# Kernel optimization log

Measured on AMD Instinct MI355X. Metric: run time of the kernel, lower is better.

Reference implementation:

```python
import jax, jax.numpy as jnp
import numpy as np

B, S, D, H, DH, TLEN, TD = 4, 1024, 1024, 16, 64, 256, 256
EPS = 1e-5


def layer_norm(x, g, b):
    m = jnp.mean(x, axis=-1, keepdims=True)
    v = jnp.mean((x - m) ** 2, axis=-1, keepdims=True)
    return (x - m) * jax.lax.rsqrt(v + EPS) * g + b


def rotate_half(x):
    x1, x2 = jnp.split(x, 2, axis=-1)
    return jnp.concatenate((-x2, x1), axis=-1)


def apply_rope(pos, t):
    # pos: [S, DH] -> [1, S, 1, DH]; t: [B, S, H, DH]
    p = pos[None, :, None, :]
    return t * jnp.cos(p) + rotate_half(t) * jnp.sin(p)


def mha(q_in, kv_in, in_w, in_b, out_w, out_b, n_heads):
    # standard nn.MultiheadAttention math (batch-first tensors here)
    d = q_in.shape[-1]
    dh = d // n_heads
    q = q_in @ in_w[:d].T + in_b[:d]
    k = kv_in @ in_w[d:2 * d].T + in_b[d:2 * d]
    v = kv_in @ in_w[2 * d:].T + in_b[2 * d:]
    q = q.reshape(q.shape[0], q.shape[1], n_heads, dh)
    k = k.reshape(k.shape[0], k.shape[1], n_heads, dh)
    v = v.reshape(v.shape[0], v.shape[1], n_heads, dh)
    scores = jnp.einsum('bihd,bjhd->bhij', q, k) / jnp.sqrt(jnp.asarray(dh, q.dtype))
    attn = jax.nn.softmax(scores, axis=-1)
    o = jnp.einsum('bhij,bjhd->bihd', attn, v)
    o = o.reshape(o.shape[0], o.shape[1], d)
    return o @ out_w.T + out_b


def setup_inputs():
    key = jax.random.key(0)
    ks = jax.random.split(key, 20)
    s = 0.02
    inp = {
        'x': jax.random.normal(ks[0], (B, S, D), jnp.float32),
        'text_emb': jax.random.normal(ks[1], (B, TLEN, D), jnp.float32),
        'time_emb': jax.random.normal(ks[2], (B, TD), jnp.float32),
    }
    # true RoPE position encoding, matching RotaryEmbedding.forward
    inv_freq = 1.0 / (10000 ** (jnp.arange(0, DH, 2, dtype=jnp.float32) / DH))
    freqs = jnp.arange(S, dtype=jnp.float32)[:, None] * inv_freq[None, :]
    inp['rotary_pos'] = jnp.concatenate((freqs, freqs), axis=-1)  # [S, DH]
    inp.update(
        ln1_g=jnp.ones((D,), jnp.float32), ln1_b=jnp.zeros((D,), jnp.float32),
        ln2_g=jnp.ones((D,), jnp.float32), ln2_b=jnp.zeros((D,), jnp.float32),
        ln3_g=jnp.ones((D,), jnp.float32), ln3_b=jnp.zeros((D,), jnp.float32),
        attn_in_w=jax.random.normal(ks[3], (3 * D, D), jnp.float32) * s,
        attn_in_b=jnp.zeros((3 * D,), jnp.float32),
        ca_in_w=jax.random.normal(ks[4], (3 * D, D), jnp.float32) * s,
        ca_in_b=jnp.zeros((3 * D,), jnp.float32),
        ca_out_w=jax.random.normal(ks[5], (D, D), jnp.float32) * s,
        ca_out_b=jnp.zeros((D,), jnp.float32),
        fc1_w=jax.random.normal(ks[6], (4 * D, D), jnp.float32) * s,
        fc1_b=jnp.zeros((4 * D,), jnp.float32),
        gate_w=jax.random.normal(ks[7], (4 * D, D), jnp.float32) * s,
        gate_b=jnp.zeros((4 * D,), jnp.float32),
        fc2_w=jax.random.normal(ks[8], (D, 4 * D), jnp.float32) * s,
        fc2_b=jnp.zeros((D,), jnp.float32),
    )
    return inp


def reference(x, text_emb, time_emb, rotary_pos,
              ln1_g, ln1_b, ln2_g, ln2_b, ln3_g, ln3_b,
              attn_in_w, attn_in_b,
              ca_in_w, ca_in_b, ca_out_w, ca_out_b,
              fc1_w, fc1_b, gate_w, gate_b, fc2_w, fc2_b):
    b, n, d = x.shape
    # --- self-attention with manual RoPE (NOTE: original skips out_proj) ---
    residual = x
    xn = layer_norm(x, ln1_g, ln1_b)
    q = xn @ attn_in_w[:d].T + attn_in_b[:d]
    k = xn @ attn_in_w[d:2 * d].T + attn_in_b[d:2 * d]
    v = xn @ attn_in_w[2 * d:].T + attn_in_b[2 * d:]
    q = q.reshape(b, n, H, DH)
    k = k.reshape(b, n, H, DH)
    v = v.reshape(b, n, H, DH)
    q = apply_rope(rotary_pos, q)
    k = apply_rope(rotary_pos, k)
    scores = jnp.einsum('bihd,bjhd->bhij', q, k) / jnp.sqrt(jnp.asarray(DH, x.dtype))
    attn = jax.nn.softmax(scores, axis=-1)
    attn_out = jnp.einsum('bhij,bjhd->bihd', attn, v).reshape(b, n, d)
    x = attn_out + residual
    # --- cross-attention (full MHA, dropout inactive at eval) ---
    residual = x
    xn = layer_norm(x, ln2_g, ln2_b)
    x = mha(xn, text_emb, ca_in_w, ca_in_b, ca_out_w, ca_out_b, H) + residual
    # --- gated MLP ---
    residual = x
    xn = layer_norm(x, ln3_g, ln3_b)
    h = jax.nn.gelu(xn @ fc1_w.T + fc1_b, approximate=False)
    g = jax.nn.sigmoid(xn @ gate_w.T + gate_b)
    return (h * g) @ fc2_w.T + fc2_b + residual
```

## Files before the change

### kernel.cpp

```cpp
#include <hip/hip_runtime.h>
#include <hip/hip_bf16.h>

#define SEQ 1024
#define DIM 1024
#define NH 16

typedef __bf16 bf16_t;
typedef __bf16 bf16x8 __attribute__((ext_vector_type(8)));
typedef __bf16 bf16x4 __attribute__((ext_vector_type(4)));
typedef float f32x4 __attribute__((ext_vector_type(4)));

__device__ __forceinline__ f32x4 mfma16(bf16x8 a, bf16x8 b, f32x4 c) {
    return __builtin_amdgcn_mfma_f32_16x16x32_bf16(a, b, c, 0, 0, 0);
}

__device__ __forceinline__ void gload16(const bf16_t* g, bf16_t* l) {
    __builtin_amdgcn_global_load_lds(
        (const __attribute__((address_space(1))) void*)g,
        (__attribute__((address_space(3))) void*)l, 16, 0, 0);
}

__global__ __launch_bounds__(256) void cvt_kernel(const float* __restrict__ in,
                                                  bf16_t* __restrict__ out) {
    const int i = blockIdx.x * 256 + threadIdx.x;
    const float4 v = ((const float4*)in)[i];
    bf16x4 o = {(bf16_t)v.x, (bf16_t)v.y, (bf16_t)v.z, (bf16_t)v.w};
    ((bf16x4*)out)[i] = o;
}

__global__ __launch_bounds__(256) void ln_kernel(const float* __restrict__ in,
                                                 const float* __restrict__ g,
                                                 const float* __restrict__ bsh,
                                                 bf16_t* __restrict__ out) {
    __shared__ float red[4], red2[4];
    const int row = blockIdx.x, tid = threadIdx.x;
    const float4 v = ((const float4*)(in + (size_t)row * DIM))[tid];
    float s = v.x + v.y + v.z + v.w;
#pragma unroll
    for (int o = 32; o; o >>= 1) s += __shfl_down(s, o, 64);
    if ((tid & 63) == 0) red[tid >> 6] = s;
    __syncthreads();
    const float mean = (red[0] + red[1] + red[2] + red[3]) * (1.0f / DIM);
    const float dx = v.x - mean, dy = v.y - mean, dz = v.z - mean, dw = v.w - mean;
    float s2 = dx * dx + dy * dy + dz * dz + dw * dw;
#pragma unroll
    for (int o = 32; o; o >>= 1) s2 += __shfl_xor(s2, o, 64);
    if ((tid & 63) == 0) red2[tid >> 6] = s2;
    __syncthreads();
    const float var = (red2[0] + red2[1] + red2[2] + red2[3]) * (1.0f / DIM);
    const float rs = rsqrtf(var + 1e-5f);
    const float4 gv = ((const float4*)g)[tid];
    const float4 bv = ((const float4*)bsh)[tid];
    bf16x4 o4 = {(bf16_t)(dx * rs * gv.x + bv.x), (bf16_t)(dy * rs * gv.y + bv.y),
                 (bf16_t)(dz * rs * gv.z + bv.z), (bf16_t)(dw * rs * gv.w + bv.w)};
    ((bf16x4*)(out + (size_t)row * DIM))[tid] = o4;
}

__global__ __launch_bounds__(256) void rope_kernel(bf16_t* __restrict__ qkv,
                                                   const float* __restrict__ rp) {
    const int t = blockIdx.x * 256 + threadIdx.x;
    const int row = t >> 9;
    const int rem = t & 511;
    const int h = rem >> 5, d = rem & 31;
    const int s = row & (SEQ - 1);
    const float p0 = rp[s * 64 + d];
    const float p1 = rp[s * 64 + d + 32];
    float s0, c0, s1, c1;
    sincosf(p0, &s0, &c0);
    sincosf(p1, &s1, &c1);
    const size_t base = (size_t)row * 3072 + h * 64 + d;
#pragma unroll
    for (int off = 0; off <= 1024; off += 1024) {
        const float a = (float)qkv[base + off];
        const float b = (float)qkv[base + off + 32];
        qkv[base + off] = (bf16_t)(a * c0 - b * s0);
        qkv[base + off + 32] = (bf16_t)(b * c1 + a * s1);
    }
}

enum { EPI_BF16 = 0, EPI_F32_RESID = 1, EPI_BF16_GELU = 2, EPI_BF16_SIGMUL = 3 };

template <int EPI>
__global__ __launch_bounds__(256) void gemm_bf16(
    const bf16_t* __restrict__ A, int lda, const bf16_t* __restrict__ W, int ldw,
    const float* __restrict__ bias, const void* __restrict__ aux,
    void* __restrict__ outv, int ldo, int K) {
    __shared__ bf16_t As[128 * 32];
    __shared__ bf16_t Bs[128 * 32];
    const int tid = threadIdx.x;
    const int wave = tid >> 6, lane = tid & 63;
    const int wr = wave >> 1, wc = wave & 1;
    const int lr = lane & 15, hi = lane >> 4;

    const int gy = gridDim.y;
    int lin = blockIdx.x * gy + blockIdx.y;
    const int cpx = (gridDim.x * gy) >> 3;
    lin = (lin & 7) * cpx + (lin >> 3);
    const int rowB0 = (lin / gy) * 128;
    const int rowA0 = (lin % gy) * 128;

    const int sr = lane >> 2, sc = (lane & 3) * 8;

    f32x4 acc[4][4];
#pragma unroll
    for (int m = 0; m < 4; ++m)
#pragma unroll
        for (int n = 0; n < 4; ++n) acc[m][n] = (f32x4){0.f, 0.f, 0.f, 0.f};

    for (int k0 = 0; k0 < K; k0 += 32) {
        const bf16_t* Ag = A + (size_t)(rowA0) * lda + k0;
        const bf16_t* Bg = W + (size_t)(rowB0) * ldw + k0;
#pragma unroll
        for (int t = 0; t < 2; ++t) {
            const int ci = wave * 2 + t;
            gload16(Ag + (size_t)(ci * 16 + sr) * lda + sc, As + ci * 512);
            gload16(Bg + (size_t)(ci * 16 + sr) * ldw + sc, Bs + ci * 512);
        }
        __syncthreads();
        bf16x8 af[4], bfr[4];
#pragma unroll
        for (int m = 0; m < 4; ++m)
            af[m] = *(const bf16x8*)&As[(wr * 64 + m * 16 + lr) * 32 + hi * 8];
#pragma unroll
        for (int n = 0; n < 4; ++n)
            bfr[n] = *(const bf16x8*)&Bs[(wc * 64 + n * 16 + lr) * 32 + hi * 8];
#pragma unroll
        for (int m = 0; m < 4; ++m)
#pragma unroll
            for (int n = 0; n < 4; ++n) acc[m][n] = mfma16(af[m], bfr[n], acc[m][n]);
        __syncthreads();
    }

    float bn[4];
#pragma unroll
    for (int n = 0; n < 4; ++n) bn[n] = bias[rowB0 + wc * 64 + n * 16 + lr];
#pragma unroll
    for (int m = 0; m < 4; ++m) {
#pragma unroll
        for (int j = 0; j < 4; ++j) {
            const int row = rowA0 + wr * 64 + m * 16 + hi * 4 + j;
#pragma unroll
            for (int n = 0; n < 4; ++n) {
                const int col = rowB0 + wc * 64 + n * 16 + lr;
                float val = acc[m][n][j] + bn[n];
                const size_t oidx = (size_t)row * ldo + col;
                if constexpr (EPI == EPI_BF16) {
                    ((bf16_t*)outv)[oidx] = (bf16_t)val;
                } else if constexpr (EPI == EPI_F32_RESID) {
                    ((float*)outv)[oidx] = val + ((const float*)aux)[oidx];
                } else if constexpr (EPI == EPI_BF16_GELU) {
                    ((bf16_t*)outv)[oidx] =
                        (bf16_t)(0.5f * val * (1.0f + erff(val * 0.70710678118f)));
                } else {
                    const float sg = 1.0f / (1.0f + expf(-val));
                    ((bf16_t*)outv)[oidx] =
                        (bf16_t)(sg * (float)((const bf16_t*)aux)[oidx]);
                }
            }
        }
    }
}

#define ALD 72
template <bool OUTBF>
__global__ __launch_bounds__(256) void attn_kernel(
    const bf16_t* __restrict__ qp, int ldq, int qoff,
    const bf16_t* __restrict__ kp, int ldk, int koff,
    const bf16_t* __restrict__ vp, int ldv, int voff, int skv,
    const float* __restrict__ resid, void* __restrict__ outp, float scale) {
    __shared__ bf16_t Ks[64 * ALD];
    __shared__ bf16_t Vt[64 * ALD];
    __shared__ bf16_t Ps[4 * 16 * ALD];
    const int b = blockIdx.z, h = blockIdx.y, qt = blockIdx.x;
    const int tid = threadIdx.x;
    const int wave = tid >> 6, lane = tid & 63;
    const int lr = lane & 15, hi = lane >> 4;

    const size_t qrow = (size_t)(b * SEQ + qt * 64 + wave * 16 + lr);
    const bf16_t* qb = qp + qrow * ldq + qoff + h * 64;
    const bf16x8 qf0 = *(const bf16x8*)(qb + hi * 8);
    const bf16x8 qf1 = *(const bf16x8*)(qb + 32 + hi * 8);

    f32x4 oacc[4];
#pragma unroll
    for (int n = 0; n < 4; ++n) oacc[n] = (f32x4){0.f, 0.f, 0.f, 0.f};
    float mrun[4] = {-1e30f, -1e30f, -1e30f, -1e30f};
    float lrun[4] = {0.f, 0.f, 0.f, 0.f};

    bf16_t* pw = &Ps[wave * 16 * ALD];
    const int nkt = skv >> 6;
    for (int kt = 0; kt < nkt; ++kt) {
#pragma unroll
        for (int t = 0; t < 2; ++t) {
            const int idx = t * 256 + tid;
            const int key = idx >> 3, c8 = (idx & 7) * 8;
            const size_t krow = (size_t)(b * skv + kt * 64 + key);
            bf16x8 kv = *(const bf16x8*)(kp + krow * ldk + koff + h * 64 + c8);
            *(bf16x8*)&Ks[key * ALD + c8] = kv;
            bf16x8 vv = *(const bf16x8*)(vp + krow * ldv + voff + h * 64 + c8);
#pragma unroll
            for (int i = 0; i < 8; ++i) Vt[(c8 + i) * ALD + key] = vv[i];
        }
        __syncthreads();

        f32x4 s[4];
#pragma unroll
        for (int n = 0; n < 4; ++n) {
            f32x4 z = (f32x4){0.f, 0.f, 0.f, 0.f};
            z = mfma16(qf0, *(const bf16x8*)&Ks[(n * 16 + lr) * ALD + hi * 8], z);
            z = mfma16(qf1, *(const bf16x8*)&Ks[(n * 16 + lr) * ALD + 32 + hi * 8], z);
            s[n] = z * scale;
        }
        float alpha[4];
#pragma unroll
        for (int j = 0; j < 4; ++j) {
            float mt = fmaxf(fmaxf(s[0][j], s[1][j]), fmaxf(s[2][j], s[3][j]));
#pragma unroll
            for (int o = 8; o >= 1; o >>= 1) mt = fmaxf(mt, __shfl_xor(mt, o, 64));
            const float mnew = fmaxf(mrun[j], mt);
            alpha[j] = expf(mrun[j] - mnew);
            float rsum = 0.f;
#pragma unroll
            for (int n = 0; n < 4; ++n) {
                const float p = expf(s[n][j] - mnew);
                s[n][j] = p;
                rsum += p;
            }
#pragma unroll
            for (int o = 8; o >= 1; o >>= 1) rsum += __shfl_xor(rsum, o, 64);
            lrun[j] = lrun[j] * alpha[j] + rsum;
            mrun[j] = mnew;
        }
#pragma unroll
        for (int j = 0; j < 4; ++j) {
            const int pr = hi * 4 + j;
#pragma unroll
            for (int n = 0; n < 4; ++n) pw[pr * ALD + n * 16 + lr] = (bf16_t)s[n][j];
        }
#pragma unroll
        for (int n = 0; n < 4; ++n)
#pragma unroll
            for (int j = 0; j < 4; ++j) oacc[n][j] *= alpha[j];
#pragma unroll
        for (int ks = 0; ks < 2; ++ks) {
            const bf16x8 pa = *(const bf16x8*)&pw[lr * ALD + ks * 32 + hi * 8];
#pragma unroll
            for (int n = 0; n < 4; ++n) {
                const bf16x8 vf = *(const bf16x8*)&Vt[(n * 16 + lr) * ALD + ks * 32 + hi * 8];
                oacc[n] = mfma16(pa, vf, oacc[n]);
            }
        }
        __syncthreads();
    }

    const size_t orow0 = (size_t)(b * SEQ + qt * 64 + wave * 16);
#pragma unroll
    for (int n = 0; n < 4; ++n) {
#pragma unroll
        for (int j = 0; j < 4; ++j) {
            const int r = hi * 4 + j;
            const size_t idx = (orow0 + r) * DIM + h * 64 + n * 16 + lr;
            float val = oacc[n][j] / lrun[j];
            if constexpr (OUTBF) {
                ((bf16_t*)outp)[idx] = (bf16_t)val;
            } else {
                ((float*)outp)[idx] = val + resid[idx];
            }
        }
    }
}

extern "C" void kernel_launch(void* const* d_in, const int* in_sizes, int n_in,
                              void* d_out, int out_size, void* d_ws, size_t ws_size,
                              hipStream_t stream) {
    const float* x = (const float*)d_in[0];
    const float* text_emb = (const float*)d_in[1];
    const float* rotary = (const float*)d_in[3];
    const float* ln1_g = (const float*)d_in[4];
    const float* ln1_b = (const float*)d_in[5];
    const float* ln2_g = (const float*)d_in[6];
    const float* ln2_b = (const float*)d_in[7];
    const float* ln3_g = (const float*)d_in[8];
    const float* ln3_b = (const float*)d_in[9];
    const float* attn_in_w = (const float*)d_in[10];
    const float* attn_in_b = (const float*)d_in[11];
    const float* ca_in_w = (const float*)d_in[12];
    const float* ca_in_b = (const float*)d_in[13];
    const float* ca_out_w = (const float*)d_in[14];
    const float* ca_out_b = (const float*)d_in[15];
    const float* fc1_w = (const float*)d_in[16];
    const float* fc1_b = (const float*)d_in[17];
    const float* gate_w = (const float*)d_in[18];
    const float* gate_b = (const float*)d_in[19];
    const float* fc2_w = (const float*)d_in[20];
    const float* fc2_b = (const float*)d_in[21];

    char* ws = (char*)d_ws;
    bf16_t* attn_w_bf = (bf16_t*)(ws);
    bf16_t* ca_in_bf = (bf16_t*)(ws + 6291456);
    bf16_t* ca_out_bf = (bf16_t*)(ws + 12582912);
    bf16_t* fc1_bf = (bf16_t*)(ws + 14680064);
    bf16_t* gate_bf = (bf16_t*)(ws + 23068672);
    bf16_t* fc2_bf = (bf16_t*)(ws + 31457280);
    bf16_t* text_bf = (bf16_t*)(ws + 39845888);
    bf16_t* xn = (bf16_t*)(ws + 41943040);
    float* xA = (float*)(ws + 50331648);
    char* S = ws + 67108864;
    bf16_t* qkv = (bf16_t*)S;
    bf16_t* cq = (bf16_t*)S;
    bf16_t* ckv = (bf16_t*)(S + 8388608);
    bf16_t* ca_attn = (bf16_t*)(S + 12582912);
    bf16_t* hbuf = (bf16_t*)S;
    float* out = (float*)d_out;

    cvt_kernel<<<3072, 256, 0, stream>>>(attn_in_w, attn_w_bf);
    cvt_kernel<<<3072, 256, 0, stream>>>(ca_in_w, ca_in_bf);
    cvt_kernel<<<1024, 256, 0, stream>>>(ca_out_w, ca_out_bf);
    cvt_kernel<<<4096, 256, 0, stream>>>(fc1_w, fc1_bf);
    cvt_kernel<<<4096, 256, 0, stream>>>(gate_w, gate_bf);
    cvt_kernel<<<4096, 256, 0, stream>>>(fc2_w, fc2_bf);
    cvt_kernel<<<1024, 256, 0, stream>>>(text_emb, text_bf);

    ln_kernel<<<4096, 256, 0, stream>>>(x, ln1_g, ln1_b, xn);
    gemm_bf16<EPI_BF16><<<dim3(24, 32), 256, 0, stream>>>(
        xn, 1024, attn_w_bf, 1024, attn_in_b, nullptr, qkv, 3072, 1024);
    rope_kernel<<<8192, 256, 0, stream>>>(qkv, rotary);
    attn_kernel<false><<<dim3(16, 16, 4), 256, 0, stream>>>(
        qkv, 3072, 0, qkv, 3072, 1024, qkv, 3072, 2048, 1024, x, xA, 0.125f);

    ln_kernel<<<4096, 256, 0, stream>>>(xA, ln2_g, ln2_b, xn);
    gemm_bf16<EPI_BF16><<<dim3(8, 32), 256, 0, stream>>>(
        xn, 1024, ca_in_bf, 1024, ca_in_b, nullptr, cq, 1024, 1024);
    gemm_bf16<EPI_BF16><<<dim3(16, 8), 256, 0, stream>>>(
        text_bf, 1024, ca_in_bf + (size_t)1024 * 1024, 1024, ca_in_b + 1024, nullptr,
        ckv, 2048, 1024);
    attn_kernel<true><<<dim3(16, 16, 4), 256, 0, stream>>>(
        cq, 1024, 0, ckv, 2048, 0, ckv, 2048, 1024, 256, nullptr, ca_attn, 0.125f);
    gemm_bf16<EPI_F32_RESID><<<dim3(8, 32), 256, 0, stream>>>(
        ca_attn, 1024, ca_out_bf, 1024, ca_out_b, xA, xA, 1024, 1024);

    ln_kernel<<<4096, 256, 0, stream>>>(xA, ln3_g, ln3_b, xn);
    gemm_bf16<EPI_BF16_GELU><<<dim3(32, 32), 256, 0, stream>>>(
        xn, 1024, fc1_bf, 1024, fc1_b, nullptr, hbuf, 4096, 1024);
    gemm_bf16<EPI_BF16_SIGMUL><<<dim3(32, 32), 256, 0, stream>>>(
        xn, 1024, gate_bf, 1024, gate_b, hbuf, hbuf, 4096, 1024);
    gemm_bf16<EPI_F32_RESID><<<dim3(8, 32), 256, 0, stream>>>(
        hbuf, 4096, fc2_bf, 4096, fc2_b, xA, out, 1024, 4096);
}
```

Measured before the change: 533.9 us.

## Add double-buffered 256x256-tile GEMM for QKV, fc1 and gate projections

Adds a gemm256 kernel with 512 threads, a 256x256 output tile, K-step 64 and double-buffered LDS staging through global_load_lds. It also raises MFMA priority with s_setprio. The existing 128-tile GEMM is changed to double-buffer its LDS tiles, so the next k-slice loads while the current one computes. The QKV, fc1 and gate projections now use the larger tile to get more data reuse per block and fewer global loads. The trade-off is fewer blocks (192 or 256) on a large-CU GPU, high register pressure from 32 accumulators per thread, and an empty stub epi_store function left in.

```diff
diff --git a/kernel.cpp b/kernel.cpp
--- a/kernel.cpp
+++ b/kernel.cpp
@@ -18,6 +18,12 @@
     __builtin_amdgcn_global_load_lds(
         (const __attribute__((address_space(1))) void*)g,
         (__attribute__((address_space(3))) void*)l, 16, 0, 0);
+}
+
+enum { EPI_BF16 = 0, EPI_F32_RESID = 1, EPI_BF16_GELU = 2, EPI_BF16_SIGMUL = 3 };
+
+__device__ __forceinline__ void epi_store(int EPI_, void* outv, size_t oidx,
+                                          float val, const void* aux) {
 }
 
 __global__ __launch_bounds__(256) void cvt_kernel(const float* __restrict__ in,
@@ -78,15 +84,13 @@
     }
 }
 
-enum { EPI_BF16 = 0, EPI_F32_RESID = 1, EPI_BF16_GELU = 2, EPI_BF16_SIGMUL = 3 };
-
 template <int EPI>
 __global__ __launch_bounds__(256) void gemm_bf16(
     const bf16_t* __restrict__ A, int lda, const bf16_t* __restrict__ W, int ldw,
     const float* __restrict__ bias, const void* __restrict__ aux,
     void* __restrict__ outv, int ldo, int K) {
-    __shared__ bf16_t As[128 * 32];
-    __shared__ bf16_t Bs[128 * 32];
+    __shared__ bf16_t As[2][4096];
+    __shared__ bf16_t Bs[2][4096];
     const int tid = threadIdx.x;
     const int wave = tid >> 6, lane = tid & 63;
     const int wr = wave >> 1, wc = wave & 1;
@@ -107,23 +111,30 @@
 #pragma unroll
         for (int n = 0; n < 4; ++n) acc[m][n] = (f32x4){0.f, 0.f, 0.f, 0.f};
 
-    for (int k0 = 0; k0 < K; k0 += 32) {
-        const bf16_t* Ag = A + (size_t)(rowA0) * lda + k0;
-        const bf16_t* Bg = W + (size_t)(rowB0) * ldw + k0;
+    auto stage = [&](int kt, int b) {
+        const bf16_t* Ag = A + (size_t)rowA0 * lda + kt * 32;
+        const bf16_t* Bg = W + (size_t)rowB0 * ldw + kt * 32;
 #pragma unroll
         for (int t = 0; t < 2; ++t) {
             const int ci = wave * 2 + t;
-            gload16(Ag + (size_t)(ci * 16 + sr) * lda + sc, As + ci * 512);
-            gload16(Bg + (size_t)(ci * 16 + sr) * ldw + sc, Bs + ci * 512);
-        }
-        __syncthreads();
+            gload16(Ag + (size_t)(ci * 16 + sr) * lda + sc, &As[b][ci * 512]);
+            gload16(Bg + (size_t)(ci * 16 + sr) * ldw + sc, &Bs[b][ci * 512]);
+        }
+    };
+
+    stage(0, 0);
+    __syncthreads();
+    const int NT = K >> 5;
+    for (int kt = 0; kt < NT; ++kt) {
+        const int b = kt & 1;
+        if (kt + 1 < NT) stage(kt + 1, b ^ 1);
         bf16x8 af[4], bfr[4];
 #pragma unroll
         for (int m = 0; m < 4; ++m)
-            af[m] = *(const bf16x8*)&As[(wr * 64 + m * 16 + lr) * 32 + hi * 8];
+            af[m] = *(const bf16x8*)&As[b][(wr * 64 + m * 16 + lr) * 32 + hi * 8];
 #pragma unroll
         for (int n = 0; n < 4; ++n)
-            bfr[n] = *(const bf16x8*)&Bs[(wc * 64 + n * 16 + lr) * 32 + hi * 8];
+            bfr[n] = *(const bf16x8*)&Bs[b][(wc * 64 + n * 16 + lr) * 32 + hi * 8];
 #pragma unroll
         for (int m = 0; m < 4; ++m)
 #pragma unroll
@@ -142,6 +153,115 @@
 #pragma unroll
             for (int n = 0; n < 4; ++n) {
                 const int col = rowB0 + wc * 64 + n * 16 + lr;
+                float val = acc[m][n][j] + bn[n];
+                const size_t oidx = (size_t)row * ldo + col;
+                if constexpr (EPI == EPI_BF16) {
+                    ((bf16_t*)outv)[oidx] = (bf16_t)val;
+                } else if constexpr (EPI == EPI_F32_RESID) {
+                    ((float*)outv)[oidx] = val + ((const float*)aux)[oidx];
+                } else if constexpr (EPI == EPI_BF16_GELU) {
+                    ((bf16_t*)outv)[oidx] =
+                        (bf16_t)(0.5f * val * (1.0f + erff(val * 0.70710678118f)));
+                } else {
+                    const float sg = 1.0f / (1.0f + expf(-val));
+                    ((bf16_t*)outv)[oidx] =
+                        (bf16_t)(sg * (float)((const bf16_t*)aux)[oidx]);
+                }
+            }
+        }
+    }
+}
+
+template <int EPI>
+__global__ __launch_bounds__(512, 1) void gemm256(
+    const bf16_t* __restrict__ A, int lda, const bf16_t* __restrict__ W, int ldw,
+    const float* __restrict__ bias, const void* __restrict__ aux,
+    void* __restrict__ outv, int ldo, int K) {
+    __shared__ bf16_t As[2][2][8192];
+    __shared__ bf16_t Bs[2][2][8192];
+    const int tid = threadIdx.x;
+    const int wave = tid >> 6, lane = tid & 63;
+    const int wm = wave >> 2, wn = wave & 3;
+    const int lr = lane & 15, hi = lane >> 4;
+
+    const int gy = gridDim.y;
+    int lin = blockIdx.x * gy + blockIdx.y;
+    const int cpx = (gridDim.x * gy) >> 3;
+    lin = (lin & 7) * cpx + (lin >> 3);
+    const int rowB0 = (lin / gy) * 256;
+    const int rowA0 = (lin % gy) * 256;
+
+    const int srow = wave * 16 + (lane >> 2);
+    const int scol = (lane & 3) * 8;
+
+    f32x4 acc[8][4];
+#pragma unroll
+    for (int m = 0; m < 8; ++m)
+#pragma unroll
+        for (int n = 0; n < 4; ++n) acc[m][n] = (f32x4){0.f, 0.f, 0.f, 0.f};
+
+    auto stage = [&](int kt, int b) {
+        const size_t koff = (size_t)kt * 64;
+#pragma unroll
+        for (int h = 0; h < 2; ++h) {
+#pragma unroll
+            for (int i = 0; i < 2; ++i) {
+                gload16(A + (size_t)(rowA0 + h * 128 + srow) * lda + koff + i * 32 + scol,
+                        &As[b][h][i * 4096 + wave * 512]);
+                gload16(W + (size_t)(rowB0 + h * 128 + srow) * ldw + koff + i * 32 + scol,
+                        &Bs[b][h][i * 4096 + wave * 512]);
+            }
+        }
+    };
+
+    stage(0, 0);
+    __syncthreads();
+    const int NT = K >> 6;
+    const int bh = wn >> 1, bg0 = (wn & 1) * 4;
+    for (int kt = 0; kt < NT; ++kt) {
+        const int b = kt & 1;
+        if (kt + 1 < NT) stage(kt + 1, b ^ 1);
+#pragma unroll
+        for (int p = 0; p < 4; ++p) {
+            const int qm = p >> 1, qn = p & 1;
+            bf16x8 af[4][2], bfr[2][2];
+#pragma unroll
+            for (int mf = 0; mf < 4; ++mf)
+#pragma unroll
+                for (int ks = 0; ks < 2; ++ks)
+                    af[mf][ks] = *(const bf16x8*)&As[b][wm][(ks * 8 + qm * 4 + mf) * 512 +
+                                                           lr * 32 + hi * 8];
+#pragma unroll
+            for (int nf = 0; nf < 2; ++nf)
+#pragma unroll
+                for (int ks = 0; ks < 2; ++ks)
+                    bfr[nf][ks] = *(const bf16x8*)&Bs[b][bh][(ks * 8 + bg0 + qn * 2 + nf) * 512 +
+                                                            lr * 32 + hi * 8];
+            __builtin_amdgcn_s_setprio(1);
+#pragma unroll
+            for (int mf = 0; mf < 4; ++mf)
+#pragma unroll
+                for (int nf = 0; nf < 2; ++nf)
+#pragma unroll
+                    for (int ks = 0; ks < 2; ++ks)
+                        acc[qm * 4 + mf][qn * 2 + nf] =
+                            mfma16(af[mf][ks], bfr[nf][ks], acc[qm * 4 + mf][qn * 2 + nf]);
+            __builtin_amdgcn_s_setprio(0);
+        }
+        __syncthreads();
+    }
+
+    float bn[4];
+#pragma unroll
+    for (int n = 0; n < 4; ++n) bn[n] = bias[rowB0 + wn * 64 + n * 16 + lr];
+#pragma unroll
+    for (int m = 0; m < 8; ++m) {
+#pragma unroll
+        for (int j = 0; j < 4; ++j) {
+            const int row = rowA0 + wm * 128 + m * 16 + hi * 4 + j;
+#pragma unroll
+            for (int n = 0; n < 4; ++n) {
+                const int col = rowB0 + wn * 64 + n * 16 + lr;
                 float val = acc[m][n][j] + bn[n];
                 const size_t oidx = (size_t)row * ldo + col;
                 if constexpr (EPI == EPI_BF16) {
@@ -322,7 +442,7 @@
     cvt_kernel<<<1024, 256, 0, stream>>>(text_emb, text_bf);
 
     ln_kernel<<<4096, 256, 0, stream>>>(x, ln1_g, ln1_b, xn);
-    gemm_bf16<EPI_BF16><<<dim3(24, 32), 256, 0, stream>>>(
+    gemm256<EPI_BF16><<<dim3(12, 16), 512, 0, stream>>>(
         xn, 1024, attn_w_bf, 1024, attn_in_b, nullptr, qkv, 3072, 1024);
     rope_kernel<<<8192, 256, 0, stream>>>(qkv, rotary);
     attn_kernel<false><<<dim3(16, 16, 4), 256, 0, stream>>>(
@@ -340,9 +460,9 @@
         ca_attn, 1024, ca_out_bf, 1024, ca_out_b, xA, xA, 1024, 1024);
 
     ln_kernel<<<4096, 256, 0, stream>>>(xA, ln3_g, ln3_b, xn);
-    gemm_bf16<EPI_BF16_GELU><<<dim3(32, 32), 256, 0, stream>>>(
+    gemm256<EPI_BF16_GELU><<<dim3(16, 16), 512, 0, stream>>>(
         xn, 1024, fc1_bf, 1024, fc1_b, nullptr, hbuf, 4096, 1024);
-    gemm_bf16<EPI_BF16_SIGMUL><<<dim3(32, 32), 256, 0, stream>>>(
+    gemm256<EPI_BF16_SIGMUL><<<dim3(16, 16), 512, 0, stream>>>(
         xn, 1024, gate_bf, 1024, gate_b, hbuf, hbuf, 4096, 1024);
     gemm_bf16<EPI_F32_RESID><<<dim3(8, 32), 256, 0, stream>>>(
         hbuf, 4096, fc2_bf, 4096, fc2_b, xA, out, 1024, 4096);
```

Result: slower. 588.7 us (+10.3%).

## Double-buffer GEMM LDS tiles with async prefetch two stages ahead

Applied to the files above, without the earlier changes.

Converts the bf16 GEMM main loop from a single LDS buffer with load-then-sync to a two-buffer pipeline. The tile two k-steps ahead is issued via global_load_lds while the current tile is consumed, with explicit vmcnt waits and barriers. It also raises wave priority around the MFMA block. The goal is to hide global-load latency behind MFMA work, at the cost of doubled LDS use and hand-managed wait counts that must match the number of outstanding loads.

```diff
diff --git a/kernel.cpp b/kernel.cpp
--- a/kernel.cpp
+++ b/kernel.cpp
@@ -19,6 +19,8 @@
         (const __attribute__((address_space(1))) void*)g,
         (__attribute__((address_space(3))) void*)l, 16, 0, 0);
 }
+
+enum { EPI_BF16 = 0, EPI_F32_RESID = 1, EPI_BF16_GELU = 2, EPI_BF16_SIGMUL = 3 };
 
 __global__ __launch_bounds__(256) void cvt_kernel(const float* __restrict__ in,
                                                   bf16_t* __restrict__ out) {
@@ -78,15 +80,13 @@
     }
 }
 
-enum { EPI_BF16 = 0, EPI_F32_RESID = 1, EPI_BF16_GELU = 2, EPI_BF16_SIGMUL = 3 };
-
 template <int EPI>
 __global__ __launch_bounds__(256) void gemm_bf16(
     const bf16_t* __restrict__ A, int lda, const bf16_t* __restrict__ W, int ldw,
     const float* __restrict__ bias, const void* __restrict__ aux,
     void* __restrict__ outv, int ldo, int K) {
-    __shared__ bf16_t As[128 * 32];
-    __shared__ bf16_t Bs[128 * 32];
+    __shared__ bf16_t As[2][4096];
+    __shared__ bf16_t Bs[2][4096];
     const int tid = threadIdx.x;
     const int wave = tid >> 6, lane = tid & 63;
     const int wr = wave >> 1, wc = wave & 1;
@@ -107,28 +107,49 @@
 #pragma unroll
         for (int n = 0; n < 4; ++n) acc[m][n] = (f32x4){0.f, 0.f, 0.f, 0.f};
 
-    for (int k0 = 0; k0 < K; k0 += 32) {
-        const bf16_t* Ag = A + (size_t)(rowA0) * lda + k0;
-        const bf16_t* Bg = W + (size_t)(rowB0) * ldw + k0;
+    auto stage = [&](int kt, int b) {
+        const bf16_t* Ag = A + (size_t)rowA0 * lda + kt * 32;
+        const bf16_t* Bg = W + (size_t)rowB0 * ldw + kt * 32;
 #pragma unroll
         for (int t = 0; t < 2; ++t) {
             const int ci = wave * 2 + t;
-            gload16(Ag + (size_t)(ci * 16 + sr) * lda + sc, As + ci * 512);
-            gload16(Bg + (size_t)(ci * 16 + sr) * ldw + sc, Bs + ci * 512);
-        }
-        __syncthreads();
+            gload16(Ag + (size_t)(ci * 16 + sr) * lda + sc, &As[b][ci * 512]);
+            gload16(Bg + (size_t)(ci * 16 + sr) * ldw + sc, &Bs[b][ci * 512]);
+        }
+    };
+
+    const int NT = K >> 5;
+    stage(0, 0);
+    stage(1, 1);
+    asm volatile("s_waitcnt vmcnt(4)" ::: "memory");
+    __builtin_amdgcn_s_barrier();
+
+    for (int kt = 0; kt < NT; ++kt) {
+        const int b = kt & 1;
         bf16x8 af[4], bfr[4];
 #pragma unroll
         for (int m = 0; m < 4; ++m)
-            af[m] = *(const bf16x8*)&As[(wr * 64 + m * 16 + lr) * 32 + hi * 8];
+            af[m] = *(const bf16x8*)&As[b][(wr * 64 + m * 16 + lr) * 32 + hi * 8];
 #pragma unroll
         for (int n = 0; n < 4; ++n)
-            bfr[n] = *(const bf16x8*)&Bs[(wc * 64 + n * 16 + lr) * 32 + hi * 8];
+            bfr[n] = *(const bf16x8*)&Bs[b][(wc * 64 + n * 16 + lr) * 32 + hi * 8];
+        __builtin_amdgcn_s_setprio(1);
 #pragma unroll
         for (int m = 0; m < 4; ++m)
 #pragma unroll
             for (int n = 0; n < 4; ++n) acc[m][n] = mfma16(af[m], bfr[n], acc[m][n]);
-        __syncthreads();
+        __builtin_amdgcn_s_setprio(0);
+        if (kt + 1 < NT) {
+            __builtin_amdgcn_sched_barrier(0);
+            __builtin_amdgcn_s_barrier();
+            if (kt + 2 < NT) {
+                stage(kt + 2, b);
+                asm volatile("s_waitcnt vmcnt(4)" ::: "memory");
+            } else {
+                asm volatile("s_waitcnt vmcnt(0)" ::: "memory");
+            }
+            __builtin_amdgcn_s_barrier();
+        }
     }
 
     float bn[4];
```

After: 574.6 us. 1.08x slower.

## Replace GEMM with 8-wave double-buffered kernel using BK=64 and fragment-friendly LDS layout

Applied to the files above, without the earlier changes.

Replaces the 4-wave 128x128 GEMM with an 8-wave version that double-buffers LDS tiles across K steps of 64, issuing the next stage's async global-to-LDS loads before computing on the current tile. This removes one barrier per iteration and overlaps memory with MFMA work. The LDS layout is also changed so each 16x32 sub-chunk matches the MFMA fragment order, and the tile swizzle becomes a 1D grid mapping. It doubles LDS use to 64KB per block and halves per-wave accumulators, which trades register pressure against occupancy. The single barrier per iteration may also race: the next stage is written into the other buffer while slow waves could still be reading it.

```diff
diff --git a/kernel.cpp b/kernel.cpp
--- a/kernel.cpp
+++ b/kernel.cpp
@@ -19,6 +19,8 @@
         (const __attribute__((address_space(1))) void*)g,
         (__attribute__((address_space(3))) void*)l, 16, 0, 0);
 }
+
+enum { EPI_BF16 = 0, EPI_F32_RESID = 1, EPI_BF16_GELU = 2, EPI_BF16_SIGMUL = 3 };
 
 __global__ __launch_bounds__(256) void cvt_kernel(const float* __restrict__ in,
                                                   bf16_t* __restrict__ out) {
@@ -78,70 +80,83 @@
     }
 }
 
-enum { EPI_BF16 = 0, EPI_F32_RESID = 1, EPI_BF16_GELU = 2, EPI_BF16_SIGMUL = 3 };
+__device__ __forceinline__ float epi_apply_gelu(float v) {
+    return 0.5f * v * (1.0f + erff(v * 0.70710678118f));
+}
 
 template <int EPI>
-__global__ __launch_bounds__(256) void gemm_bf16(
+__global__ __launch_bounds__(512, 4) void gemm8w(
     const bf16_t* __restrict__ A, int lda, const bf16_t* __restrict__ W, int ldw,
     const float* __restrict__ bias, const void* __restrict__ aux,
-    void* __restrict__ outv, int ldo, int K) {
-    __shared__ bf16_t As[128 * 32];
-    __shared__ bf16_t Bs[128 * 32];
+    void* __restrict__ outv, int ldo, int K, int nM) {
+    __shared__ bf16_t As[2][8192];
+    __shared__ bf16_t Bs[2][8192];
     const int tid = threadIdx.x;
     const int wave = tid >> 6, lane = tid & 63;
-    const int wr = wave >> 1, wc = wave & 1;
+    const int wm = wave >> 2, wn = wave & 3;
     const int lr = lane & 15, hi = lane >> 4;
 
-    const int gy = gridDim.y;
-    int lin = blockIdx.x * gy + blockIdx.y;
-    const int cpx = (gridDim.x * gy) >> 3;
-    lin = (lin & 7) * cpx + (lin >> 3);
-    const int rowB0 = (lin / gy) * 128;
-    const int rowA0 = (lin % gy) * 128;
-
-    const int sr = lane >> 2, sc = (lane & 3) * 8;
-
-    f32x4 acc[4][4];
+    const int q = gridDim.x >> 3;
+    const int t = (blockIdx.x & 7) * q + (blockIdx.x >> 3);
+    const int rowA0 = (t % nM) * 128;
+    const int rowB0 = (t / nM) * 128;
+
+    f32x4 acc[4][2];
 #pragma unroll
     for (int m = 0; m < 4; ++m)
 #pragma unroll
-        for (int n = 0; n < 4; ++n) acc[m][n] = (f32x4){0.f, 0.f, 0.f, 0.f};
-
-    for (int k0 = 0; k0 < K; k0 += 32) {
-        const bf16_t* Ag = A + (size_t)(rowA0) * lda + k0;
-        const bf16_t* Bg = W + (size_t)(rowB0) * ldw + k0;
-#pragma unroll
-        for (int t = 0; t < 2; ++t) {
-            const int ci = wave * 2 + t;
-            gload16(Ag + (size_t)(ci * 16 + sr) * lda + sc, As + ci * 512);
-            gload16(Bg + (size_t)(ci * 16 + sr) * ldw + sc, Bs + ci * 512);
+        for (int n = 0; n < 2; ++n) acc[m][n] = (f32x4){0.f, 0.f, 0.f, 0.f};
+
+    const int c0 = wave * 2;
+    auto stage = [&](int kt, int b) {
+        const int k0 = kt * 64;
+#pragma unroll
+        for (int u = 0; u < 2; ++u) {
+            const int c = c0 + u, s = c >> 1, ks = c & 1;
+            const int grow = s * 16 + lr, gcol = k0 + ks * 32 + hi * 8;
+            gload16(A + (size_t)(rowA0 + grow) * lda + gcol, &As[b][c * 512]);
+            gload16(W + (size_t)(rowB0 + grow) * ldw + gcol, &Bs[b][c * 512]);
+        }
+    };
+
+    const int NT = K >> 6;
+    stage(0, 0);
+    __syncthreads();
+
+    for (int kt = 0; kt < NT; ++kt) {
+        const int cur = kt & 1;
+        if (kt + 1 < NT) stage(kt + 1, cur ^ 1);
+#pragma unroll
+        for (int ks = 0; ks < 2; ++ks) {
+            bf16x8 af[4], bfr[2];
+#pragma unroll
+            for (int mf = 0; mf < 4; ++mf)
+                af[mf] = *(const bf16x8*)&As[cur][((wm * 4 + mf) * 2 + ks) * 512 +
+                                                 hi * 128 + lr * 8];
+#pragma unroll
+            for (int nf = 0; nf < 2; ++nf)
+                bfr[nf] = *(const bf16x8*)&Bs[cur][((wn * 2 + nf) * 2 + ks) * 512 +
+                                                  hi * 128 + lr * 8];
+#pragma unroll
+            for (int mf = 0; mf < 4; ++mf)
+#pragma unroll
+                for (int nf = 0; nf < 2; ++nf)
+                    acc[mf][nf] = mfma16(af[mf], bfr[nf], acc[mf][nf]);
         }
         __syncthreads();
-        bf16x8 af[4], bfr[4];
-#pragma unroll
-        for (int m = 0; m < 4; ++m)
-            af[m] = *(const bf16x8*)&As[(wr * 64 + m * 16 + lr) * 32 + hi * 8];
-#pragma unroll
-        for (int n = 0; n < 4; ++n)
-            bfr[n] = *(const bf16x8*)&Bs[(wc * 64 + n * 16 + lr) * 32 + hi * 8];
-#pragma unroll
-        for (int m = 0; m < 4; ++m)
-#pragma unroll
-            for (int n = 0; n < 4; ++n) acc[m][n] = mfma16(af[m], bfr[n], acc[m][n]);
-        __syncthreads();
-    }
-
-    float bn[4];
-#pragma unroll
-    for (int n = 0; n < 4; ++n) bn[n] = bias[rowB0 + wc * 64 + n * 16 + lr];
+    }
+
+    float bn[2];
+#pragma unroll
+    for (int n = 0; n < 2; ++n) bn[n] = bias[rowB0 + wn * 32 + n * 16 + lr];
 #pragma unroll
     for (int m = 0; m < 4; ++m) {
 #pragma unroll
         for (int j = 0; j < 4; ++j) {
-            const int row = rowA0 + wr * 64 + m * 16 + hi * 4 + j;
-#pragma unroll
-            for (int n = 0; n < 4; ++n) {
-                const int col = rowB0 + wc * 64 + n * 16 + lr;
+            const int row = rowA0 + wm * 64 + m * 16 + hi * 4 + j;
+#pragma unroll
+            for (int n = 0; n < 2; ++n) {
+                const int col = rowB0 + wn * 32 + n * 16 + lr;
                 float val = acc[m][n][j] + bn[n];
                 const size_t oidx = (size_t)row * ldo + col;
                 if constexpr (EPI == EPI_BF16) {
@@ -149,8 +164,7 @@
                 } else if constexpr (EPI == EPI_F32_RESID) {
                     ((float*)outv)[oidx] = val + ((const float*)aux)[oidx];
                 } else if constexpr (EPI == EPI_BF16_GELU) {
-                    ((bf16_t*)outv)[oidx] =
-                        (bf16_t)(0.5f * val * (1.0f + erff(val * 0.70710678118f)));
+                    ((bf16_t*)outv)[oidx] = (bf16_t)epi_apply_gelu(val);
                 } else {
                     const float sg = 1.0f / (1.0f + expf(-val));
                     ((bf16_t*)outv)[oidx] =
@@ -322,28 +336,28 @@
     cvt_kernel<<<1024, 256, 0, stream>>>(text_emb, text_bf);
 
     ln_kernel<<<4096, 256, 0, stream>>>(x, ln1_g, ln1_b, xn);
-    gemm_bf16<EPI_BF16><<<dim3(24, 32), 256, 0, stream>>>(
-        xn, 1024, attn_w_bf, 1024, attn_in_b, nullptr, qkv, 3072, 1024);
+    gemm8w<EPI_BF16><<<768, 512, 0, stream>>>(
+        xn, 1024, attn_w_bf, 1024, attn_in_b, nullptr, qkv, 3072, 1024, 32);
     rope_kernel<<<8192, 256, 0, stream>>>(qkv, rotary);
     attn_kernel<false><<<dim3(16, 16, 4), 256, 0, stream>>>(
         qkv, 3072, 0, qkv, 3072, 1024, qkv, 3072, 2048, 1024, x, xA, 0.125f);
 
     ln_kernel<<<4096, 256, 0, stream>>>(xA, ln2_g, ln2_b, xn);
-    gemm_bf16<EPI_BF16><<<dim3(8, 32), 256, 0, stream>>>(
-        xn, 1024, ca_in_bf, 1024, ca_in_b, nullptr, cq, 1024, 1024);
-    gemm_bf16<EPI_BF16><<<dim3(16, 8), 256, 0, stream>>>(
+    gemm8w<EPI_BF16><<<256, 512, 0, stream>>>(
+        xn, 1024, ca_in_bf, 1024, ca_in_b, nullptr, cq, 1024, 1024, 32);
+    gemm8w<EPI_BF16><<<128, 512, 0, stream>>>(
         text_bf, 1024, ca_in_bf + (size_t)1024 * 1024, 1024, ca_in_b + 1024, nullptr,
-        ckv, 2048, 1024);
+        ckv, 2048, 1024, 8);
     attn_kernel<true><<<dim3(16, 16, 4), 256, 0, stream>>>(
         cq, 1024, 0, ckv, 2048, 0, ckv, 2048, 1024, 256, nullptr, ca_attn, 0.125f);
-    gemm_bf16<EPI_F32_RESID><<<dim3(8, 32), 256, 0, stream>>>(
-        ca_attn, 1024, ca_out_bf, 1024, ca_out_b, xA, xA, 1024, 1024);
+    gemm8w<EPI_F32_RESID><<<256, 512, 0, stream>>>(
+        ca_attn, 1024, ca_out_bf, 1024, ca_out_b, xA, xA, 1024, 1024, 32);
 
     ln_kernel<<<4096, 256, 0, stream>>>(xA, ln3_g, ln3_b, xn);
-    gemm_bf16<EPI_BF16_GELU><<<dim3(32, 32), 256, 0, stream>>>(
-        xn, 1024, fc1_bf, 1024, fc1_b, nullptr, hbuf, 4096, 1024);
-    gemm_bf16<EPI_BF16_SIGMUL><<<dim3(32, 32), 256, 0, stream>>>(
-        xn, 1024, gate_bf, 1024, gate_b, hbuf, hbuf, 4096, 1024);
-    gemm_bf16<EPI_F32_RESID><<<dim3(8, 32), 256, 0, stream>>>(
-        hbuf, 4096, fc2_bf, 4096, fc2_b, xA, out, 1024, 4096);
-}
+    gemm8w<EPI_BF16_GELU><<<1024, 512, 0, stream>>>(
+        xn, 1024, fc1_bf, 1024, fc1_b, nullptr, hbuf, 4096, 1024, 32);
+    gemm8w<EPI_BF16_SIGMUL><<<1024, 512, 0, stream>>>(
+        xn, 1024, gate_bf, 1024, gate_b, hbuf, hbuf, 4096, 1024, 32);
+    gemm8w<EPI_F32_RESID><<<256, 512, 0, stream>>>(
+        hbuf, 4096, fc2_bf, 4096, fc2_b, xA, out, 1024, 4096, 32);
+}
```

After: 569.8 us. 6.7% more time.
